# Performance work log

Hardware: AMD Instinct MI355X
Metric: run time of the kernel (lower is better)

## Reference

```python
import jax, jax.numpy as jnp
import numpy as np

N, T, D, E1 = 64, 32, 128, 128
EPS = 1e-6


def _mlp(x, W1, b1, W2, b2):
    # Linear -> ReLU -> (Dropout: identity in eval) -> Linear
    return jnp.maximum(x @ W1 + b1, 0.0) @ W2 + b2


def _forward(x_time, x_news,
             it_W1, it_b1, it_W2, it_b2,
             inw_W1, inw_b1, inw_W2, inw_b2,
             t2n_W1, t2n_b1, t2n_W2, t2n_b2,
             n2t_W1, n2t_b1, n2t_W2, n2t_b2,
             f_W1, f_b1, f_W2, f_b2,
             theta_t, theta_n):
    xt = x_time.reshape(-1, D)   # [NT, D]
    xn = x_news.reshape(-1, D)   # [NT, D]

    # incidence-matrix candidates, each [NT, E1]
    H_time = xt @ _mlp(xt.T, it_W1, it_b1, it_W2, it_b2)
    H_news = xn @ _mlp(xn.T, inw_W1, inw_b1, inw_W2, inw_b2)
    H_t2n = xt @ _mlp(xn.T, t2n_W1, t2n_b1, t2n_W2, t2n_b2)
    H_n2t = xn @ _mlp(xt.T, n2t_W1, n2t_b1, n2t_W2, n2t_b2)

    H = _mlp(jnp.concatenate([H_time, H_news, H_t2n, H_n2t], axis=1),
             f_W1, f_b1, f_W2, f_b2)  # [NT, E1]

    # column-wise standardization (torch.std is unbiased -> ddof=1) + softmax over nodes
    H = (H - H.mean(axis=0, keepdims=True)) / (H.std(axis=0, ddof=1, keepdims=True) + EPS)
    H = jax.nn.softmax(H, axis=0)

    # pairwise Jensen-Shannon divergence between columns of H -> [E1, E1]
    logH = jnp.log(H)
    M = (H[:, :, None] + H[:, None, :]) * 0.5          # [NT, E1, E1]
    kl_pm = jnp.sum(H[:, :, None] * (logH[:, :, None] - jnp.log(M)), axis=0)  # KL(P||M)
    # KL(Q||M)[i,j] == KL(P||M)[j,i] since M is symmetric in (i,j)
    jsd = (kl_pm + kl_pm.T) * 0.5

    jm = jsd.mean(axis=0)                               # [E1]
    njm = (jm - jm.mean()) / (jm.std(ddof=1) + EPS)
    w = jax.nn.softmax(njm)                             # diagonal of hyperedge weight W

    # Hypergraph conv with residual: x + elu(H @ diag(w) @ H.T @ x @ theta)
    # reassociated (exactly equal math) to avoid the O((NT)^2) intermediate
    Hw = H * w[None, :]                                 # [NT, E1]
    xt = xt + jax.nn.elu(Hw @ (H.T @ (xt @ theta_t)))
    xn = xn + jax.nn.elu(Hw @ (H.T @ (xn @ theta_n)))

    return xt.reshape(N, T, D), xn.reshape(N, T, D)


def setup_inputs() -> dict:
    key = jax.random.key(0)
    ks = iter(jax.random.split(key, 32))
    NT = N * T

    def lin(i, o):
        return (jax.random.normal(next(ks), (i, o), jnp.float32) / np.float32(np.sqrt(i)))

    inp = {
        "x_time": jax.random.normal(next(ks), (N, T, D), jnp.float32),
        "x_news": jax.random.normal(next(ks), (N, T, D), jnp.float32),
    }
    for pre in ["it", "inw", "t2n", "n2t"]:
        inp[pre + "_W1"] = lin(NT, E1)
        inp[pre + "_b1"] = jnp.zeros((E1,), jnp.float32)
        inp[pre + "_W2"] = lin(E1, E1)
        inp[pre + "_b2"] = jnp.zeros((E1,), jnp.float32)
    inp["f_W1"] = lin(4 * E1, E1)
    inp["f_b1"] = jnp.zeros((E1,), jnp.float32)
    inp["f_W2"] = lin(E1, E1)
    inp["f_b2"] = jnp.zeros((E1,), jnp.float32)
    # HypergraphConvolution uses torch.randn init for theta
    inp["theta_t"] = jax.random.normal(next(ks), (D, D), jnp.float32)
    inp["theta_n"] = jax.random.normal(next(ks), (D, D), jnp.float32)
    return inp


def reference(x_time, x_news,
              it_W1, it_b1, it_W2, it_b2,
              inw_W1, inw_b1, inw_W2, inw_b2,
              t2n_W1, t2n_b1, t2n_W2, t2n_b2,
              n2t_W1, n2t_b1, n2t_W2, n2t_b2,
              f_W1, f_b1, f_W2, f_b2,
              theta_t, theta_n):
    return _forward(x_time, x_news,
                    it_W1, it_b1, it_W2, it_b2,
                    inw_W1, inw_b1, inw_W2, inw_b2,
                    t2n_W1, t2n_b1, t2n_W2, t2n_b2,
                    n2t_W1, n2t_b1, n2t_W2, n2t_b2,
                    f_W1, f_b1, f_W2, f_b2,
                    theta_t, theta_n)
```

## Files before the change

### kernel.cpp

```cpp
#include <hip/hip_runtime.h>
#include <hip/hip_bf16.h>
#include <math.h>

#define NTOT 2048
#define DIM  128
#define MSPLIT 8
#define ZSPLIT 8
#define JT 16
#define JNC 128
#define JNSPLIT 8

struct P4 { const float* p[4]; };

__global__ __launch_bounds__(256) void gk_mlp1t(P4 X, P4 W1, float* __restrict__ Gs) {
  int k = blockIdx.z;
  int m0 = (blockIdx.x & 3) * 32;
  int e0 = (blockIdx.x >> 2) * 32;
  int split = blockIdx.y;
  int n0 = split * (NTOT / MSPLIT);
  const float* Xp = X.p[k];
  const float* Wp = W1.p[k];
  __shared__ float Xs[32][36], Ws[32][36];
  int tid = threadIdx.x;
  int lr = tid >> 3;
  int lc = (tid & 7) * 4;
  int tx = tid & 15, ty = tid >> 4;
  float a00 = 0.f, a01 = 0.f, a10 = 0.f, a11 = 0.f;
  long g0 = (long)(n0 + lr) * DIM;
  float4 xv = *(const float4*)(Xp + g0 + m0 + lc);
  float4 wv = *(const float4*)(Wp + g0 + e0 + lc);
  for (int nb = 0; nb < NTOT / MSPLIT; nb += 32) {
    *(float4*)&Xs[lr][lc] = xv;
    *(float4*)&Ws[lr][lc] = wv;
    __syncthreads();
    if (nb + 32 < NTOT / MSPLIT) {
      long gn = (long)(n0 + nb + 32 + lr) * DIM;
      xv = *(const float4*)(Xp + gn + m0 + lc);
      wv = *(const float4*)(Wp + gn + e0 + lc);
    }
    #pragma unroll
    for (int nn = 0; nn < 32; ++nn) {
      float x0 = Xs[nn][2*ty], x1 = Xs[nn][2*ty+1];
      float w0 = Ws[nn][2*tx], w1 = Ws[nn][2*tx+1];
      a00 += x0 * w0; a01 += x0 * w1;
      a10 += x1 * w0; a11 += x1 * w1;
    }
    __syncthreads();
  }
  float* Gk = Gs + ((long)k * MSPLIT + split) * 16384;
  int m = m0 + 2 * ty, e = e0 + 2 * tx;
  Gk[m * DIM + e]           = a00;
  Gk[m * DIM + e + 1]       = a01;
  Gk[(m + 1) * DIM + e]     = a10;
  Gk[(m + 1) * DIM + e + 1] = a11;
}

__global__ __launch_bounds__(256) void gk_mab(const float* __restrict__ Gs, P4 B1, P4 W2, P4 B2,
                                              const float* __restrict__ fW1, float* __restrict__ AB) {
  int m = blockIdx.x;
  int e = threadIdx.x & 127;
  int half = threadIdx.x >> 7;
  int k0 = half, k1 = half + 2;
  __shared__ float rk[4][DIM];
  __shared__ float mk[4][DIM];
  {
    const float* G0 = Gs + (long)k0 * MSPLIT * 16384 + m * DIM + e;
    const float* G1 = Gs + (long)k1 * MSPLIT * 16384 + m * DIM + e;
    float s0 = 0.f, s1 = 0.f;
    #pragma unroll
    for (int s = 0; s < MSPLIT; ++s) { s0 += G0[s * 16384]; s1 += G1[s * 16384]; }
    rk[k0][e] = fmaxf(s0 + B1.p[k0][e], 0.f);
    rk[k1][e] = fmaxf(s1 + B1.p[k1][e], 0.f);
  }
  __syncthreads();
  {
    const float* Wa = W2.p[k0];
    const float* Wb = W2.p[k1];
    float a0 = B2.p[k0][e], a1 = B2.p[k1][e];
    #pragma unroll 8
    for (int j = 0; j < DIM; ++j) {
      a0 += rk[k0][j] * Wa[j * DIM + e];
      a1 += rk[k1][j] * Wb[j * DIM + e];
    }
    mk[k0][e] = a0;
    mk[k1][e] = a1;
  }
  __syncthreads();
  const float* Ma = mk[half];
  const float* Mb = mk[half + 2];
  const float* W0 = fW1 + (half == 0 ? 0 : 128) * DIM;
  const float* W1p = fW1 + (half == 0 ? 256 : 384) * DIM;
  float acc = 0.f;
  #pragma unroll 8
  for (int j = 0; j < DIM; ++j)
    acc += Ma[j] * W0[j * DIM + e] + Mb[j] * W1p[j * DIM + e];
  AB[(long)half * 16384 + m * DIM + e] = acc;
}

__global__ __launch_bounds__(256) void gk_h12t(const float* __restrict__ xt, const float* __restrict__ xn,
                                               const float* __restrict__ AB, const float* __restrict__ fb1,
                                               const float* __restrict__ fW2, const float* __restrict__ fb2,
                                               float* __restrict__ HrawT) {
  int n0 = blockIdx.x * 8;
  int e  = threadIdx.x & 127;
  int rr = (threadIdx.x >> 7) << 2;
  __shared__ float stT[DIM][8], snT[DIM][8], h1T[DIM][8];
  {
    int c = threadIdx.x & 31, rq = threadIdx.x >> 5;
    const float* xtr = xt + (long)(n0 + rq) * DIM;
    const float* xnr = xn + (long)(n0 + rq) * DIM;
    #pragma unroll
    for (int i = 0; i < 4; ++i) {
      int d = c + 32 * i;
      stT[d][rq] = xtr[d];
      snT[d][rq] = xnr[d];
    }
  }
  __syncthreads();
  float4 acc1 = make_float4(0.f, 0.f, 0.f, 0.f);
  #pragma unroll 8
  for (int k = 0; k < DIM; ++k) {
    float a = AB[k * DIM + e];
    float b = AB[16384 + k * DIM + e];
    const float4 xv = *(const float4*)&stT[k][rr];
    const float4 nv = *(const float4*)&snT[k][rr];
    acc1.x += xv.x * a + nv.x * b;
    acc1.y += xv.y * a + nv.y * b;
    acc1.z += xv.z * a + nv.z * b;
    acc1.w += xv.w * a + nv.w * b;
  }
  float b1v = fb1[e];
  float4 h1;
  h1.x = fmaxf(acc1.x + b1v, 0.f);
  h1.y = fmaxf(acc1.y + b1v, 0.f);
  h1.z = fmaxf(acc1.z + b1v, 0.f);
  h1.w = fmaxf(acc1.w + b1v, 0.f);
  *(float4*)&h1T[e][rr] = h1;
  __syncthreads();
  float4 acc2 = make_float4(0.f, 0.f, 0.f, 0.f);
  #pragma unroll 8
  for (int j = 0; j < DIM; ++j) {
    float wv = fW2[j * DIM + e];
    const float4 hv = *(const float4*)&h1T[j][rr];
    acc2.x += hv.x * wv;
    acc2.y += hv.y * wv;
    acc2.z += hv.z * wv;
    acc2.w += hv.w * wv;
  }
  float b2v = fb2[e];
  float4 o;
  o.x = acc2.x + b2v; o.y = acc2.y + b2v; o.z = acc2.z + b2v; o.w = acc2.w + b2v;
  *(float4*)&HrawT[(long)e * NTOT + n0 + rr] = o;
}

__global__ __launch_bounds__(256) void colsoft_k(const float* __restrict__ HrawT,
                                                 float* __restrict__ HTp, float* __restrict__ Ecol,
                                                 float* __restrict__ Gacc) {
  int e = blockIdx.x;
  int t = threadIdx.x;
  if (e == 0 && t < DIM) Gacc[t] = 0.f;
  __shared__ float sa[4], sb[4], sc[4];
  float v[8];
  float sum = 0.f, sq = 0.f, mx = -3.4e38f;
  #pragma unroll
  for (int r = 0; r < 8; ++r) {
    float x = HrawT[(long)e * NTOT + t + 256 * r];
    v[r] = x;
    sum += x; sq += x * x; mx = fmaxf(mx, x);
  }
  #pragma unroll
  for (int o = 32; o > 0; o >>= 1) {
    sum += __shfl_down(sum, o);
    sq  += __shfl_down(sq, o);
    mx   = fmaxf(mx, __shfl_down(mx, o));
  }
  if ((t & 63) == 0) { int w = t >> 6; sa[w] = sum; sb[w] = sq; sc[w] = mx; }
  __syncthreads();
  sum = sa[0] + sa[1] + sa[2] + sa[3];
  sq  = sb[0] + sb[1] + sb[2] + sb[3];
  mx  = fmaxf(fmaxf(sc[0], sc[1]), fmaxf(sc[2], sc[3]));
  float mean = sum * (1.f / NTOT);
  float var  = (sq - sum * mean) * (1.f / (NTOT - 1));
  float ia   = 1.f / (sqrtf(fmaxf(var, 0.f)) + 1e-6f);
  float smax = (mx - mean) * ia;
  __syncthreads();

  float den = 0.f;
  #pragma unroll
  for (int r = 0; r < 8; ++r) {
    float s = (v[r] - mean) * ia - smax;
    v[r] = s;
    den += __expf(s);
  }
  #pragma unroll
  for (int o = 32; o > 0; o >>= 1) den += __shfl_down(den, o);
  if ((t & 63) == 0) sa[t >> 6] = den;
  __syncthreads();
  den = sa[0] + sa[1] + sa[2] + sa[3];
  float logden = __logf(den);
  float invden = 1.f / den;
  __syncthreads();

  float ent = 0.f;
  #pragma unroll
  for (int r = 0; r < 8; ++r) {
    float s = v[r];
    float pv = __expf(s) * invden;
    HTp[(long)e * NTOT + t + 256 * r] = pv;
    ent += pv * (s - logden);
  }
  #pragma unroll
  for (int o = 32; o > 0; o >>= 1) ent += __shfl_down(ent, o);
  if ((t & 63) == 0) sa[t >> 6] = ent;
  __syncthreads();
  if (t == 0) Ecol[e] = sa[0] + sa[1] + sa[2] + sa[3];
}

__global__ __launch_bounds__(256) void jsd_tile(const float* __restrict__ HTp,
                                                float* __restrict__ g) {
  int b = blockIdx.x;
  int bi = 0, rem = b;
  while (rem >= 8 - bi) { rem -= 8 - bi; ++bi; }
  int bj = bi + rem;
  int n0 = blockIdx.y * (NTOT / JNSPLIT);

  __shared__ float Ti[JT][JNC + 2];
  __shared__ float Tj[JT][JNC + 2];
  __shared__ float red[JT][JT + 1];

  int tid = threadIdx.x;
  int ti = tid >> 4, tj = tid & 15;
  bool active = (bi != bj) || (ti < tj);
  float acc = 0.f;

  int lc = tid >> 4;
  int ln = (tid & 15) * 8;

  for (int c = 0; c < NTOT / JNSPLIT; c += JNC) {
    const float* si = HTp + (long)(bi * JT + lc) * NTOT + n0 + c + ln;
    const float* sj = HTp + (long)(bj * JT + lc) * NTOT + n0 + c + ln;
    #pragma unroll
    for (int r = 0; r < 8; ++r) Ti[lc][ln + r] = si[r];
    #pragma unroll
    for (int r = 0; r < 8; ++r) Tj[lc][ln + r] = sj[r];
    __syncthreads();
    if (active) {
      #pragma unroll 4
      for (int n = 0; n < JNC; ++n) {
        float s = Ti[ti][n] + Tj[tj][n];
        acc += s * __logf(fmaxf(0.5f * s, 1e-38f));
      }
    }
    __syncthreads();
  }

  red[ti][tj] = active ? acc : 0.f;
  __syncthreads();
  if (tid < JT) {
    float s = 0.f;
    #pragma unroll
    for (int j = 0; j < JT; ++j) s += red[tid][j];
    atomicAdd(&g[bi * JT + tid], -s);
  } else if (tid < 2 * JT) {
    int c2 = tid - JT;
    float s = 0.f;
    #pragma unroll
    for (int i = 0; i < JT; ++i) s += red[i][c2];
    atomicAdd(&g[bj * JT + c2], -s);
  }
}

__global__ __launch_bounds__(256) void xz_k(const float* __restrict__ HTp, const float* __restrict__ xt,
                                            const float* __restrict__ xn, float* __restrict__ Xzs) {
  int bt = blockIdx.z;
  const float* x = bt ? xn : xt;
  int split = blockIdx.y;
  float* C = Xzs + ((long)bt * ZSPLIT + split) * 16384;
  int e0 = (blockIdx.x & 3) * 32, d0 = (blockIdx.x >> 2) * 32;
  int n0 = split * (NTOT / ZSPLIT);
  __shared__ float As[32][33], Bs[32][36];
  int tid = threadIdx.x, col = tid & 31, row = tid >> 5;
  int lr = tid >> 3, lc4 = (tid & 7) * 4;
  int tx = tid & 15, ty = tid >> 4;
  float a00 = 0.f, a01 = 0.f, a10 = 0.f, a11 = 0.f;
  float pa[4]; float4 pb;
  #pragma unroll
  for (int r = 0; r < 4; ++r) pa[r] = HTp[(long)(e0 + row + r * 8) * NTOT + n0 + col];
  pb = *(const float4*)(x + (long)(n0 + lr) * DIM + d0 + lc4);
  for (int nb = 0; nb < NTOT / ZSPLIT; nb += 32) {
    #pragma unroll
    for (int r = 0; r < 4; ++r) As[col][row + r * 8] = pa[r];
    *(float4*)&Bs[lr][lc4] = pb;
    __syncthreads();
    if (nb + 32 < NTOT / ZSPLIT) {
      #pragma unroll
      for (int r = 0; r < 4; ++r)
        pa[r] = HTp[(long)(e0 + row + r * 8) * NTOT + n0 + nb + 32 + col];
      pb = *(const float4*)(x + (long)(n0 + nb + 32 + lr) * DIM + d0 + lc4);
    }
    #pragma unroll
    for (int nn = 0; nn < 32; ++nn) {
      float e0v = As[nn][2*ty], e1v = As[nn][2*ty+1];
      float d0v = Bs[nn][2*tx], d1v = Bs[nn][2*tx+1];
      a00 += e0v * d0v; a01 += e0v * d1v;
      a10 += e1v * d0v; a11 += e1v * d1v;
    }
    __syncthreads();
  }
  int e = e0 + 2 * ty, d = d0 + 2 * tx;
  C[e * DIM + d]           = a00;
  C[e * DIM + d + 1]       = a01;
  C[(e + 1) * DIM + d]     = a10;
  C[(e + 1) * DIM + d + 1] = a11;
}

__global__ __launch_bounds__(128) void zs_k(const float* __restrict__ Xzs, const float* __restrict__ thT,
                                            const float* __restrict__ thN, const float* __restrict__ g,
                                            const float* __restrict__ Ecol, float* __restrict__ Zw) {
  int e = blockIdx.x, d = threadIdx.x, bt = blockIdx.y;
  __shared__ float s2[2];
  __shared__ float swv;
  int t = d;
  float ec = Ecol[t];
  float v = ec;
  #pragma unroll
  for (int o = 32; o > 0; o >>= 1) v += __shfl_down(v, o);
  if ((t & 63) == 0) s2[t >> 6] = v;
  __syncthreads();
  float S = s2[0] + s2[1];
  __syncthreads();
  float jm = (g[t] + 126.f * ec + S) * (1.0f / 256.0f);
  v = jm;
  #pragma unroll
  for (int o = 32; o > 0; o >>= 1) v += __shfl_down(v, o);
  if ((t & 63) == 0) s2[t >> 6] = v;
  __syncthreads();
  float mean = (s2[0] + s2[1]) * (1.0f / 128.0f);
  __syncthreads();
  float dv = jm - mean;
  v = dv * dv;
  #pragma unroll
  for (int o = 32; o > 0; o >>= 1) v += __shfl_down(v, o);
  if ((t & 63) == 0) s2[t >> 6] = v;
  __syncthreads();
  float var = (s2[0] + s2[1]) * (1.0f / 127.0f);
  float njm = dv / (sqrtf(var) + 1e-6f);
  __syncthreads();
  v = njm;
  #pragma unroll
  for (int o = 32; o > 0; o >>= 1) v = fmaxf(v, __shfl_down(v, o));
  if ((t & 63) == 0) s2[t >> 6] = v;
  __syncthreads();
  float mx = fmaxf(s2[0], s2[1]);
  float ex = __expf(njm - mx);
  __syncthreads();
  v = ex;
  #pragma unroll
  for (int o = 32; o > 0; o >>= 1) v += __shfl_down(v, o);
  if ((t & 63) == 0) s2[t >> 6] = v;
  __syncthreads();
  if (t == e) swv = ex / (s2[0] + s2[1]);
  __syncthreads();
  float we = swv;

  const float* src = Xzs + (long)bt * ZSPLIT * 16384 + e * DIM + d;
  const float* th = bt ? thN : thT;
  __shared__ float s[DIM];
  float xv = 0.f;
  #pragma unroll
  for (int sp = 0; sp < ZSPLIT; ++sp) xv += src[sp * 16384];
  s[d] = xv;
  __syncthreads();
  float acc = 0.f;
  #pragma unroll 8
  for (int k = 0; k < DIM; ++k) acc += s[k] * th[(long)k * DIM + d];
  Zw[bt * 16384 + e * DIM + d] = acc * we;
}

__global__ __launch_bounds__(256) void uk_t(const float* __restrict__ HTp, const float* __restrict__ Zw,
                                            const float* __restrict__ xt, const float* __restrict__ xn,
                                            float* __restrict__ out) {
  int bt = blockIdx.z;
  const float* x = bt ? xn : xt;
  const float* B = Zw + bt * 16384;
  float* o = out + (long)bt * NTOT * DIM;
  int d0 = blockIdx.x * 32, n0 = blockIdx.y * 32;
  __shared__ float As[32][33], Bs[32][36];
  int tid = threadIdx.x, col = tid & 31, row = tid >> 5;
  int lr = tid >> 3, lc4 = (tid & 7) * 4;
  int tx = tid & 15, ty = tid >> 4;
  float a00 = 0.f, a01 = 0.f, a10 = 0.f, a11 = 0.f;
  float pa[4]; float4 pb;
  #pragma unroll
  for (int r = 0; r < 4; ++r) pa[r] = HTp[(long)(row + r * 8) * NTOT + n0 + col];
  pb = *(const float4*)(B + (long)lr * DIM + d0 + lc4);
  for (int eb = 0; eb < DIM; eb += 32) {
    #pragma unroll
    for (int r = 0; r < 4; ++r) As[col][row + r * 8] = pa[r];
    *(float4*)&Bs[lr][lc4] = pb;
    __syncthreads();
    if (eb + 32 < DIM) {
      #pragma unroll
      for (int r = 0; r < 4; ++r)
        pa[r] = HTp[(long)(eb + 32 + row + r * 8) * NTOT + n0 + col];
      pb = *(const float4*)(B + (long)(eb + 32 + lr) * DIM + d0 + lc4);
    }
    #pragma unroll
    for (int ee = 0; ee < 32; ++ee) {
      float x0 = As[2*ty][ee], x1 = As[2*ty+1][ee];
      float b0 = Bs[ee][2*tx], b1 = Bs[ee][2*tx+1];
      a00 += x0 * b0; a01 += x0 * b1;
      a10 += x1 * b0; a11 += x1 * b1;
    }
    __syncthreads();
  }
  int n = n0 + 2 * ty, d = d0 + 2 * tx;
  long i0 = (long)n * DIM + d, i1 = i0 + DIM;
  float e00 = a00 > 0.f ? a00 : expm1f(a00);
  float e01 = a01 > 0.f ? a01 : expm1f(a01);
  float e10 = a10 > 0.f ? a10 : expm1f(a10);
  float e11 = a11 > 0.f ? a11 : expm1f(a11);
  o[i0]     = x[i0]     + e00;
  o[i0 + 1] = x[i0 + 1] + e01;
  o[i1]     = x[i1]     + e10;
  o[i1 + 1] = x[i1 + 1] + e11;
}

extern "C" void kernel_launch(void* const* d_in, const int* in_sizes, int n_in,
                              void* d_out, int out_size, void* d_ws, size_t ws_size,
                              hipStream_t stream) {
  const float* xt = (const float*)d_in[0];
  const float* xn = (const float*)d_in[1];
  const float *W1[4], *b1[4], *W2[4], *b2[4];
  for (int k = 0; k < 4; ++k) {
    W1[k] = (const float*)d_in[2 + 4*k];
    b1[k] = (const float*)d_in[3 + 4*k];
    W2[k] = (const float*)d_in[4 + 4*k];
    b2[k] = (const float*)d_in[5 + 4*k];
  }
  const float* fW1 = (const float*)d_in[18];
  const float* fb1 = (const float*)d_in[19];
  const float* fW2 = (const float*)d_in[20];
  const float* fb2 = (const float*)d_in[21];
  const float* thT = (const float*)d_in[22];
  const float* thN = (const float*)d_in[23];

  float* ws    = (float*)d_ws;
  float* Gacc  = ws;
  float* Ecol  = ws + 128;
  float* Zw    = ws + 384;
  float* Xzs   = ws + 33152;
  float* Gs    = ws + 295296;
  float* AB    = ws + 885120;
  float* HrawT = ws + 917888;
  float* HTp   = ws + 1180032;

  float* out = (float*)d_out;

  P4 Xs  = {{xt, xn, xn, xt}};
  P4 W1s = {{W1[0], W1[1], W1[2], W1[3]}};
  P4 B1s = {{b1[0], b1[1], b1[2], b1[3]}};
  P4 W2s = {{W2[0], W2[1], W2[2], W2[3]}};
  P4 B2s = {{b2[0], b2[1], b2[2], b2[3]}};

  gk_mlp1t<<<dim3(16, MSPLIT, 4), 256, 0, stream>>>(Xs, W1s, Gs);
  gk_mab  <<<128, 256, 0, stream>>>(Gs, B1s, W2s, B2s, fW1, AB);
  gk_h12t <<<256, 256, 0, stream>>>(xt, xn, AB, fb1, fW2, fb2, HrawT);

  colsoft_k<<<DIM, 256, 0, stream>>>(HrawT, HTp, Ecol, Gacc);

  jsd_tile<<<dim3(36, JNSPLIT), 256, 0, stream>>>(HTp, Gacc);

  xz_k<<<dim3(16, ZSPLIT, 2), 256, 0, stream>>>(HTp, xt, xn, Xzs);
  zs_k<<<dim3(128, 2), 128, 0, stream>>>(Xzs, thT, thN, Gacc, Ecol, Zw);
  uk_t<<<dim3(4, 64, 2), 256, 0, stream>>>(HTp, Zw, xt, xn, out);

  (void)in_sizes; (void)n_in; (void)out_size; (void)ws_size;
}
```

Baseline: 183.8 us.

## Merge JSD and H^T·x kernels into one launch, double split factors, warp-level weight softmax

The JSD tile kernel and the H^T·x partial GEMM kernel are combined into a single launch that dispatches on block index, with their shared-memory tiles overlaid in a union. MSPLIT, ZSPLIT and JNSPLIT are doubled so each kernel issues more, smaller blocks, and the workspace offsets move to hold the larger partial buffers. zs_k now computes the hyperedge-weight softmax inside one wavefront with xor shuffles instead of repeated block reductions and barriers. This removes one launch and adds parallelism, at the cost of more partial sums and more atomics.

```diff
diff --git a/kernel.cpp b/kernel.cpp
--- a/kernel.cpp
+++ b/kernel.cpp
@@ -4,11 +4,11 @@
 
 #define NTOT 2048
 #define DIM  128
-#define MSPLIT 8
-#define ZSPLIT 8
+#define MSPLIT 16
+#define ZSPLIT 16
 #define JT 16
 #define JNC 128
-#define JNSPLIT 8
+#define JNSPLIT 16
 
 struct P4 { const float* p[4]; };
 
@@ -216,153 +216,134 @@
   if (t == 0) Ecol[e] = sa[0] + sa[1] + sa[2] + sa[3];
 }
 
-__global__ __launch_bounds__(256) void jsd_tile(const float* __restrict__ HTp,
-                                                float* __restrict__ g) {
-  int b = blockIdx.x;
-  int bi = 0, rem = b;
-  while (rem >= 8 - bi) { rem -= 8 - bi; ++bi; }
-  int bj = bi + rem;
-  int n0 = blockIdx.y * (NTOT / JNSPLIT);
-
-  __shared__ float Ti[JT][JNC + 2];
-  __shared__ float Tj[JT][JNC + 2];
-  __shared__ float red[JT][JT + 1];
-
+__global__ __launch_bounds__(256) void jx_k(const float* __restrict__ HTp,
+                                            const float* __restrict__ xt, const float* __restrict__ xn,
+                                            float* __restrict__ g, float* __restrict__ Xzs) {
+  __shared__ union {
+    struct { float Ti[JT][JNC + 2], Tj[JT][JNC + 2], red[JT][JT + 1]; } j;
+    struct { float As[32][33], Bs[32][36]; } x;
+  } sm;
+  int bid = blockIdx.x;
   int tid = threadIdx.x;
-  int ti = tid >> 4, tj = tid & 15;
-  bool active = (bi != bj) || (ti < tj);
-  float acc = 0.f;
-
-  int lc = tid >> 4;
-  int ln = (tid & 15) * 8;
-
-  for (int c = 0; c < NTOT / JNSPLIT; c += JNC) {
-    const float* si = HTp + (long)(bi * JT + lc) * NTOT + n0 + c + ln;
-    const float* sj = HTp + (long)(bj * JT + lc) * NTOT + n0 + c + ln;
-    #pragma unroll
-    for (int r = 0; r < 8; ++r) Ti[lc][ln + r] = si[r];
-    #pragma unroll
-    for (int r = 0; r < 8; ++r) Tj[lc][ln + r] = sj[r];
-    __syncthreads();
+
+  if (bid < 576) {
+    int ny = bid / 36, b = bid - ny * 36;
+    int bi = 0, rem = b;
+    while (rem >= 8 - bi) { rem -= 8 - bi; ++bi; }
+    int bj = bi + rem;
+    int n0 = ny * (NTOT / JNSPLIT);
+    int ti = tid >> 4, tj = tid & 15;
+    bool active = (bi != bj) || (ti < tj);
+    int lc = tid >> 4, ln = (tid & 15) * 8;
+    const float* si = HTp + (long)(bi * JT + lc) * NTOT + n0 + ln;
+    const float* sj = HTp + (long)(bj * JT + lc) * NTOT + n0 + ln;
+    #pragma unroll
+    for (int r = 0; r < 8; ++r) sm.j.Ti[lc][ln + r] = si[r];
+    #pragma unroll
+    for (int r = 0; r < 8; ++r) sm.j.Tj[lc][ln + r] = sj[r];
+    __syncthreads();
+    float acc = 0.f;
     if (active) {
       #pragma unroll 4
       for (int n = 0; n < JNC; ++n) {
-        float s = Ti[ti][n] + Tj[tj][n];
+        float s = sm.j.Ti[ti][n] + sm.j.Tj[tj][n];
         acc += s * __logf(fmaxf(0.5f * s, 1e-38f));
       }
     }
-    __syncthreads();
-  }
-
-  red[ti][tj] = active ? acc : 0.f;
-  __syncthreads();
-  if (tid < JT) {
-    float s = 0.f;
-    #pragma unroll
-    for (int j = 0; j < JT; ++j) s += red[tid][j];
-    atomicAdd(&g[bi * JT + tid], -s);
-  } else if (tid < 2 * JT) {
-    int c2 = tid - JT;
-    float s = 0.f;
-    #pragma unroll
-    for (int i = 0; i < JT; ++i) s += red[i][c2];
-    atomicAdd(&g[bj * JT + c2], -s);
-  }
-}
-
-__global__ __launch_bounds__(256) void xz_k(const float* __restrict__ HTp, const float* __restrict__ xt,
-                                            const float* __restrict__ xn, float* __restrict__ Xzs) {
-  int bt = blockIdx.z;
-  const float* x = bt ? xn : xt;
-  int split = blockIdx.y;
-  float* C = Xzs + ((long)bt * ZSPLIT + split) * 16384;
-  int e0 = (blockIdx.x & 3) * 32, d0 = (blockIdx.x >> 2) * 32;
-  int n0 = split * (NTOT / ZSPLIT);
-  __shared__ float As[32][33], Bs[32][36];
-  int tid = threadIdx.x, col = tid & 31, row = tid >> 5;
-  int lr = tid >> 3, lc4 = (tid & 7) * 4;
-  int tx = tid & 15, ty = tid >> 4;
-  float a00 = 0.f, a01 = 0.f, a10 = 0.f, a11 = 0.f;
-  float pa[4]; float4 pb;
-  #pragma unroll
-  for (int r = 0; r < 4; ++r) pa[r] = HTp[(long)(e0 + row + r * 8) * NTOT + n0 + col];
-  pb = *(const float4*)(x + (long)(n0 + lr) * DIM + d0 + lc4);
-  for (int nb = 0; nb < NTOT / ZSPLIT; nb += 32) {
-    #pragma unroll
-    for (int r = 0; r < 4; ++r) As[col][row + r * 8] = pa[r];
-    *(float4*)&Bs[lr][lc4] = pb;
-    __syncthreads();
-    if (nb + 32 < NTOT / ZSPLIT) {
+    sm.j.red[ti][tj] = active ? acc : 0.f;
+    __syncthreads();
+    if (tid < JT) {
+      float s = 0.f;
       #pragma unroll
-      for (int r = 0; r < 4; ++r)
-        pa[r] = HTp[(long)(e0 + row + r * 8) * NTOT + n0 + nb + 32 + col];
-      pb = *(const float4*)(x + (long)(n0 + nb + 32 + lr) * DIM + d0 + lc4);
-    }
-    #pragma unroll
-    for (int nn = 0; nn < 32; ++nn) {
-      float e0v = As[nn][2*ty], e1v = As[nn][2*ty+1];
-      float d0v = Bs[nn][2*tx], d1v = Bs[nn][2*tx+1];
-      a00 += e0v * d0v; a01 += e0v * d1v;
-      a10 += e1v * d0v; a11 += e1v * d1v;
-    }
-    __syncthreads();
-  }
-  int e = e0 + 2 * ty, d = d0 + 2 * tx;
-  C[e * DIM + d]           = a00;
-  C[e * DIM + d + 1]       = a01;
-  C[(e + 1) * DIM + d]     = a10;
-  C[(e + 1) * DIM + d + 1] = a11;
+      for (int q = 0; q < JT; ++q) s += sm.j.red[tid][q];
+      atomicAdd(&g[bi * JT + tid], -s);
+    } else if (tid < 2 * JT) {
+      int c2 = tid - JT;
+      float s = 0.f;
+      #pragma unroll
+      for (int i = 0; i < JT; ++i) s += sm.j.red[i][c2];
+      atomicAdd(&g[bj * JT + c2], -s);
+    }
+  } else {
+    int id = bid - 576;
+    int bt = id >> 8;
+    int split = (id >> 4) & 15;
+    int t16 = id & 15;
+    const float* x = bt ? xn : xt;
+    float* C = Xzs + ((long)bt * ZSPLIT + split) * 16384;
+    int e0 = (t16 & 3) * 32, d0 = (t16 >> 2) * 32;
+    int n0 = split * (NTOT / ZSPLIT);
+    int col = tid & 31, row = tid >> 5;
+    int lr = tid >> 3, lc4 = (tid & 7) * 4;
+    int tx = tid & 15, ty = tid >> 4;
+    float a00 = 0.f, a01 = 0.f, a10 = 0.f, a11 = 0.f;
+    float pa[4]; float4 pb;
+    #pragma unroll
+    for (int r = 0; r < 4; ++r) pa[r] = HTp[(long)(e0 + row + r * 8) * NTOT + n0 + col];
+    pb = *(const float4*)(x + (long)(n0 + lr) * DIM + d0 + lc4);
+    for (int nb = 0; nb < NTOT / ZSPLIT; nb += 32) {
+      #pragma unroll
+      for (int r = 0; r < 4; ++r) sm.x.As[col][row + r * 8] = pa[r];
+      *(float4*)&sm.x.Bs[lr][lc4] = pb;
+      __syncthreads();
+      if (nb + 32 < NTOT / ZSPLIT) {
+        #pragma unroll
+        for (int r = 0; r < 4; ++r)
+          pa[r] = HTp[(long)(e0 + row + r * 8) * NTOT + n0 + nb + 32 + col];
+        pb = *(const float4*)(x + (long)(n0 + nb + 32 + lr) * DIM + d0 + lc4);
+      }
+      #pragma unroll
+      for (int nn = 0; nn < 32; ++nn) {
+        float e0v = sm.x.As[nn][2*ty], e1v = sm.x.As[nn][2*ty+1];
+        float d0v = sm.x.Bs[nn][2*tx], d1v = sm.x.Bs[nn][2*tx+1];
+        a00 += e0v * d0v; a01 += e0v * d1v;
+        a10 += e1v * d0v; a11 += e1v * d1v;
+      }
+      __syncthreads();
+    }
+    int e = e0 + 2 * ty, d = d0 + 2 * tx;
+    C[e * DIM + d]           = a00;
+    C[e * DIM + d + 1]       = a01;
+    C[(e + 1) * DIM + d]     = a10;
+    C[(e + 1) * DIM + d + 1] = a11;
+  }
 }
 
 __global__ __launch_bounds__(128) void zs_k(const float* __restrict__ Xzs, const float* __restrict__ thT,
                                             const float* __restrict__ thN, const float* __restrict__ g,
                                             const float* __restrict__ Ecol, float* __restrict__ Zw) {
   int e = blockIdx.x, d = threadIdx.x, bt = blockIdx.y;
-  __shared__ float s2[2];
-  __shared__ float swv;
-  int t = d;
-  float ec = Ecol[t];
-  float v = ec;
-  #pragma unroll
-  for (int o = 32; o > 0; o >>= 1) v += __shfl_down(v, o);
-  if ((t & 63) == 0) s2[t >> 6] = v;
-  __syncthreads();
-  float S = s2[0] + s2[1];
-  __syncthreads();
-  float jm = (g[t] + 126.f * ec + S) * (1.0f / 256.0f);
-  v = jm;
-  #pragma unroll
-  for (int o = 32; o > 0; o >>= 1) v += __shfl_down(v, o);
-  if ((t & 63) == 0) s2[t >> 6] = v;
-  __syncthreads();
-  float mean = (s2[0] + s2[1]) * (1.0f / 128.0f);
-  __syncthreads();
-  float dv = jm - mean;
-  v = dv * dv;
-  #pragma unroll
-  for (int o = 32; o > 0; o >>= 1) v += __shfl_down(v, o);
-  if ((t & 63) == 0) s2[t >> 6] = v;
-  __syncthreads();
-  float var = (s2[0] + s2[1]) * (1.0f / 127.0f);
-  float njm = dv / (sqrtf(var) + 1e-6f);
-  __syncthreads();
-  v = njm;
-  #pragma unroll
-  for (int o = 32; o > 0; o >>= 1) v = fmaxf(v, __shfl_down(v, o));
-  if ((t & 63) == 0) s2[t >> 6] = v;
-  __syncthreads();
-  float mx = fmaxf(s2[0], s2[1]);
-  float ex = __expf(njm - mx);
-  __syncthreads();
-  v = ex;
-  #pragma unroll
-  for (int o = 32; o > 0; o >>= 1) v += __shfl_down(v, o);
-  if ((t & 63) == 0) s2[t >> 6] = v;
-  __syncthreads();
-  if (t == e) swv = ex / (s2[0] + s2[1]);
-  __syncthreads();
-  float we = swv;
-
+  float we;
+  {
+    int l = threadIdx.x & 63;
+    float gA = g[l], gB = g[l + 64];
+    float eA = Ecol[l], eB = Ecol[l + 64];
+    float S = eA + eB;
+    #pragma unroll
+    for (int o = 32; o > 0; o >>= 1) S += __shfl_xor(S, o);
+    float jA = (gA + 126.f * eA + S) * (1.f / 256.f);
+    float jB = (gB + 126.f * eB + S) * (1.f / 256.f);
+    float sn = jA + jB;
+    #pragma unroll
+    for (int o = 32; o > 0; o >>= 1) sn += __shfl_xor(sn, o);
+    float mean = sn * (1.f / 128.f);
+    float dA = jA - mean, dB = jB - mean;
+    float q = dA * dA + dB * dB;
+    #pragma unroll
+    for (int o = 32; o > 0; o >>= 1) q += __shfl_xor(q, o);
+    float inv = 1.f / (sqrtf(q * (1.f / 127.f)) + 1e-6f);
+    float nA = dA * inv, nB = dB * inv;
+    float mx = fmaxf(nA, nB);
+    #pragma unroll
+    for (int o = 32; o > 0; o >>= 1) mx = fmaxf(mx, __shfl_xor(mx, o));
+    float xA = __expf(nA - mx), xB = __expf(nB - mx);
+    float den = xA + xB;
+    #pragma unroll
+    for (int o = 32; o > 0; o >>= 1) den += __shfl_xor(den, o);
+    float sel = (e < 64) ? nA : nB;
+    float ne = __shfl(sel, e & 63);
+    we = __expf(ne - mx) / den;
+  }
   const float* src = Xzs + (long)bt * ZSPLIT * 16384 + e * DIM + d;
   const float* th = bt ? thN : thT;
   __shared__ float s[DIM];
@@ -450,10 +431,10 @@
   float* Ecol  = ws + 128;
   float* Zw    = ws + 384;
   float* Xzs   = ws + 33152;
-  float* Gs    = ws + 295296;
-  float* AB    = ws + 885120;
-  float* HrawT = ws + 917888;
-  float* HTp   = ws + 1180032;
+  float* Gs    = ws + 557440;
+  float* AB    = ws + 1606016;
+  float* HrawT = ws + 1638784;
+  float* HTp   = ws + 1900928;
 
   float* out = (float*)d_out;
 
@@ -469,9 +450,8 @@
 
   colsoft_k<<<DIM, 256, 0, stream>>>(HrawT, HTp, Ecol, Gacc);
 
-  jsd_tile<<<dim3(36, JNSPLIT), 256, 0, stream>>>(HTp, Gacc);
-
-  xz_k<<<dim3(16, ZSPLIT, 2), 256, 0, stream>>>(HTp, xt, xn, Xzs);
+  jx_k<<<576 + 512, 256, 0, stream>>>(HTp, xt, xn, Gacc, Xzs);
+
   zs_k<<<dim3(128, 2), 128, 0, stream>>>(Xzs, thT, thN, Gacc, Ecol, Zw);
   uk_t<<<dim3(4, 64, 2), 256, 0, stream>>>(HTp, Zw, xt, xn, out);
 
```

Measured after the change: 177.2 us. 3.6% less time.
